# Kernel optimization log

Measured on AMD Instinct MI355X. Metric: run time of the kernel, lower is better.

The kernel has to match this reference:

```python
import jax, jax.numpy as jnp
import numpy as np
import math

N, E = 50000, 800000
N_BASIS, N_ATOM, L = 32, 128, 2
START, STOP = 0.0, 10.0

_idx = [(i, j, L - i - j) for i in range(L + 1) for j in range(L + 1 - i)]
IP = np.array([t[0] for t in _idx], np.float32)
JP = np.array([t[1] for t in _idx], np.float32)
KP = np.array([t[2] for t in _idx], np.float32)
_d = np.array([math.factorial(a) * math.factorial(b) * math.factorial(c) for a, b, c in _idx], np.float32)
PREF2 = np.sqrt(math.factorial(L) / _d).astype(np.float32)  # [T], T = (L+1)(L+2)/2 = 6
OFFSETS = np.linspace(START, STOP, N_BASIS, dtype=np.float32)
WIDTH = np.float32(OFFSETS[1] - OFFSETS[0])


def _signed_pow(x, p):
    # matches torch.pow for negative base with integer-valued float exponent
    p = np.asarray(p)
    odd = (p.astype(np.int64) % 2 == 1)
    r = jnp.abs(x)[:, None] ** jnp.asarray(p)[None, :]
    return jnp.where((x < 0.0)[:, None] & jnp.asarray(odd)[None, :], -r, r)


def setup_inputs() -> dict:
    key = jax.random.key(0)
    ks = jax.random.split(key, 12)
    s = 0.05
    return {
        "feat": jax.random.normal(ks[0], (N, N_ATOM), jnp.float32),
        "dis_vec": jax.random.normal(ks[1], (E, 3), jnp.float32),
        "cj_w1": jax.random.normal(ks[2], (N_ATOM, N_ATOM), jnp.float32) * s,
        "cj_b1": jnp.zeros((N_ATOM,), jnp.float32),
        "cj_w2": jax.random.normal(ks[3], (N_ATOM, 1), jnp.float32) * s,
        "cj_b2": jnp.zeros((1,), jnp.float32),
        "msg_w1": jax.random.normal(ks[4], (N_BASIS, N_ATOM), jnp.float32) * s,
        "msg_b1": jnp.zeros((N_ATOM,), jnp.float32),
        "msg_w2": jax.random.normal(ks[5], (N_ATOM, N_ATOM), jnp.float32) * s,
        "msg_b2": jnp.zeros((N_ATOM,), jnp.float32),
        "filt_w1": jax.random.normal(ks[6], (IP.shape[0], IP.shape[0]), jnp.float32) * s,
        "filt_w2": jax.random.normal(ks[7], (IP.shape[0], 1), jnp.float32) * s,
        "filt_b2": jnp.zeros((1,), jnp.float32),
        "src": jax.random.randint(ks[8], (E,), 0, N, jnp.int32),
        "dst": jax.random.randint(ks[9], (E,), 0, N, jnp.int32),
    }


def reference(feat, dis_vec, cj_w1, cj_b1, cj_w2, cj_b2, msg_w1, msg_b1, msg_w2, msg_b2, filt_w1, filt_w2, filt_b2, src, dst):
    silu = jax.nn.silu  # swish
    # polynomial prefactor: [E, T]
    phix = _signed_pow(dis_vec[:, 0] + 1e-8, IP)
    phiy = _signed_pow(dis_vec[:, 1] + 1e-8, JP)
    phiz = _signed_pow(dis_vec[:, 2] + 1e-8, KP)
    prefactor = phix * phiy * phiz
    # gaussian basis: [E, n_basis] (cutoff_network is None -> C = 1)
    dis = jnp.linalg.norm(dis_vec + 1e-9, axis=-1)
    coeff = -0.5 / (WIDTH ** 2)
    g0 = jnp.exp(coeff * (dis[:, None] - jnp.asarray(OFFSETS)[None, :]) ** 2)
    # gauss: [E, n_basis, T]
    gauss = prefactor[:, None, :] * g0[:, :, None] * jnp.asarray(PREF2)[None, None, :]
    # cj = cj_mlp(feat): [N, 1]
    cj = silu(feat @ cj_w1 + cj_b1) @ cj_w2 + cj_b2
    # e_mul_v: gather dst-node scalar onto edges; copy_e_sum(g.reverse()): scatter-sum to src nodes
    fij = gauss * cj[dst][:, :, None]  # [E, n_basis, T]
    agg = jax.ops.segment_sum(fij, src, num_segments=N)  # [N, n_basis, T]
    f2 = jnp.sum(agg ** 2, axis=-1)  # [N, n_basis]
    msg_in = f2 / (jnp.linalg.norm(f2 + 1e-9, axis=-1, keepdims=True) + 1.0)
    msg_out = silu(msg_in @ msg_w1 + msg_b1) @ msg_w2 + msg_b2  # [N, n_atom_basis]
    gn = gauss / (jnp.linalg.norm(gauss + 1e-8, axis=-1) + 1.0)[..., None]
    filt = (silu(gn @ filt_w1) @ filt_w2 + filt_b2)[..., 0]  # [E, n_basis]
    return msg_out, filt
```

## Files before the change

kernel.cpp:

```cpp
#include <hip/hip_runtime.h>
#include <math.h>

#define N_NODES 50000
#define N_EDGES 800000
#define NB 32
#define NA 128
#define CJ_BLOCKS 782
#define CNT_BLOCKS 3125
#define EDGE_BLOCKS 3125
#define SCAN_BLOCKS 49

constexpr double STEP_D = 10.0 / 31.0;
constexpr float  STEP_F = (float)(10.0 / 31.0);
constexpr float  COEFF  = -0.5f / (STEP_F * STEP_F);
constexpr float  R2     = 1.41421356237309515f;
constexpr float  INV_STEP = 3.1f;
constexpr float  HWIN   = 2.05f;

__device__ __forceinline__ float fast_rcp(float x) {
    return __builtin_amdgcn_rcpf(x);
}

__device__ __forceinline__ float silu_f(float x) {
    return x * fast_rcp(1.0f + __expf(-x));
}

__global__ __launch_bounds__(256) void k_cj_count(const float* __restrict__ feat,
                                                  const float* __restrict__ w1,
                                                  const float* __restrict__ b1,
                                                  const float* __restrict__ w2,
                                                  const float* __restrict__ b2,
                                                  float* __restrict__ cj,
                                                  const int* __restrict__ src,
                                                  int* __restrict__ cnt) {
    __shared__ float fls[64 * 128];
    int tid = threadIdx.x;
    int blk = blockIdx.x;
    if (blk >= CJ_BLOCKS) {
        int e = (blk - CJ_BLOCKS) * 256 + tid;
        if (e < N_EDGES) atomicAdd(&cnt[src[e]], 1);
        return;
    }
    int jq  = tid & 31;
    int ng  = tid >> 5;
    int j0  = jq * 4;
    int n0  = blk * 64;

    {
        const float4* fp = (const float4*)feat;
        int base = n0 * 32;
        int maxi = N_NODES * 32 - 1;
#pragma unroll
        for (int r = 0; r < 8; r++) {
            int idx = base + r * 256 + tid;
            ((float4*)fls)[r * 256 + tid] = fp[min(idx, maxi)];
        }
    }
    __syncthreads();

    float4 bv = *(const float4*)&b1[j0];
    float h[8][4];
#pragma unroll
    for (int i = 0; i < 8; i++) {
        h[i][0] = bv.x; h[i][1] = bv.y; h[i][2] = bv.z; h[i][3] = bv.w;
    }
    for (int kb = 0; kb < 128; kb += 4) {
        float4 wv[4];
#pragma unroll
        for (int u = 0; u < 4; u++) wv[u] = *(const float4*)&w1[(kb + u) * 128 + j0];
#pragma unroll
        for (int i = 0; i < 8; i++) {
            float4 f4 = *(const float4*)&fls[(ng * 8 + i) * 128 + kb];
            h[i][0] = fmaf(f4.x, wv[0].x, h[i][0]);
            h[i][1] = fmaf(f4.x, wv[0].y, h[i][1]);
            h[i][2] = fmaf(f4.x, wv[0].z, h[i][2]);
            h[i][3] = fmaf(f4.x, wv[0].w, h[i][3]);
            h[i][0] = fmaf(f4.y, wv[1].x, h[i][0]);
            h[i][1] = fmaf(f4.y, wv[1].y, h[i][1]);
            h[i][2] = fmaf(f4.y, wv[1].z, h[i][2]);
            h[i][3] = fmaf(f4.y, wv[1].w, h[i][3]);
            h[i][0] = fmaf(f4.z, wv[2].x, h[i][0]);
            h[i][1] = fmaf(f4.z, wv[2].y, h[i][1]);
            h[i][2] = fmaf(f4.z, wv[2].z, h[i][2]);
            h[i][3] = fmaf(f4.z, wv[2].w, h[i][3]);
            h[i][0] = fmaf(f4.w, wv[3].x, h[i][0]);
            h[i][1] = fmaf(f4.w, wv[3].y, h[i][1]);
            h[i][2] = fmaf(f4.w, wv[3].z, h[i][2]);
            h[i][3] = fmaf(f4.w, wv[3].w, h[i][3]);
        }
    }
    float4 w2v = *(const float4*)&w2[j0];
    float keep = 0.f;
#pragma unroll
    for (int i = 0; i < 8; i++) {
        float v = silu_f(h[i][0]) * w2v.x + silu_f(h[i][1]) * w2v.y
                + silu_f(h[i][2]) * w2v.z + silu_f(h[i][3]) * w2v.w;
#pragma unroll
        for (int m = 1; m < 32; m <<= 1) v += __shfl_xor(v, m, 64);
        if (jq == i) keep = v;
    }
    if (jq < 8) {
        int n = n0 + ng * 8 + jq;
        if (n < N_NODES) cj[n] = b2[0] + keep;
    }
}

__global__ __launch_bounds__(1024) void k_scan(const int* __restrict__ cnt,
                                               int* __restrict__ offs,
                                               int* __restrict__ cursor,
                                               int* __restrict__ bsum) {
    __shared__ int s[1024];
    __shared__ int sbase;
    int bid = blockIdx.x;
    int i = bid * 1024 + threadIdx.x;
    int v = (i < N_NODES) ? cnt[i] : 0;
    s[threadIdx.x] = v;
    __syncthreads();
    for (int o = 1; o < 1024; o <<= 1) {
        int t = (threadIdx.x >= (unsigned)o) ? s[threadIdx.x - o] : 0;
        __syncthreads();
        s[threadIdx.x] += t;
        __syncthreads();
    }
    if (threadIdx.x == 1023) atomicExch(&bsum[bid], s[1023] + 1);
    if (threadIdx.x < 64) {
        int lane = threadIdx.x;
        int val = 0;
        if (lane < bid) {
            int t;
            do { t = atomicAdd(&bsum[lane], 0); } while (t == 0);
            val = t - 1;
        }
#pragma unroll
        for (int m = 1; m < 64; m <<= 1) val += __shfl_xor(val, m, 64);
        if (lane == 0) sbase = val;
    }
    __syncthreads();
    if (i < N_NODES) {
        int o2 = s[threadIdx.x] - v + sbase;
        offs[i] = o2;
        cursor[i] = o2;
    }
}

__global__ __launch_bounds__(256) void k_edge(const int* __restrict__ src,
                                              const int* __restrict__ dst,
                                              const float* __restrict__ dis_vec,
                                              const float* __restrict__ cj,
                                              int* __restrict__ cursor,
                                              float* __restrict__ sedge,
                                              const float* __restrict__ fw1,
                                              const float* __restrict__ fw2,
                                              const float* __restrict__ fb2,
                                              float* __restrict__ outf) {
    __shared__ float buf[256 * 36];
    int tid = threadIdx.x;
    int e = blockIdx.x * 256 + tid;
    int se = src[e];
    int de = dst[e];
    float dx = dis_vec[3 * e], dy = dis_vec[3 * e + 1], dz = dis_vec[3 * e + 2];
    float cjd = cj[de];
    int p = atomicAdd(&cursor[se], 1);

    float ax = dx + 1e-9f, ay = dy + 1e-9f, az = dz + 1e-9f;
    float dis = sqrtf(ax * ax + ay * ay + az * az);
    float x = dx + 1e-8f, y = dy + 1e-8f, z = dz + 1e-8f;
    float pre[6];
    pre[0] = z * z;      pre[1] = y * z * R2; pre[2] = y * y;
    pre[3] = x * z * R2; pre[4] = x * y * R2; pre[5] = x * x;

    {
        float4* op = (float4*)(sedge + (size_t)p * 8);
        op[0] = make_float4(dis, pre[0] * cjd, pre[1] * cjd, pre[2] * cjd);
        op[1] = make_float4(pre[3] * cjd, pre[4] * cjd, pre[5] * cjd, 0.f);
    }

    float A = 0.f, B = 0.f;
#pragma unroll
    for (int t = 0; t < 6; t++) { A = fmaf(pre[t], pre[t], A); B += pre[t]; }
    float q[6];
#pragma unroll
    for (int tp = 0; tp < 6; tp++) {
        float s = 0.f;
#pragma unroll
        for (int t = 0; t < 6; t++) s = fmaf(pre[t], fw1[t * 6 + tp], s);
        q[tp] = s;
    }
    float bias = fb2[0];
    float w2r[6];
#pragma unroll
    for (int t = 0; t < 6; t++) w2r[t] = fw2[t];

    float* row = &buf[tid * 36];
    float4 b4v = make_float4(bias, bias, bias, bias);
#pragma unroll
    for (int r = 0; r < 8; r++) ((float4*)row)[r] = b4v;

    int b_lo = (int)ceilf((dis - HWIN) * INV_STEP);
#pragma unroll
    for (int k = 0; k < 14; k++) {
        int b = b_lo + k;
        float offb = (float)((double)b * STEP_D);
        float dd = dis - offb;
        float g = __expf(COEFF * dd * dd);
        float ns = fmaf(g * g, A, fmaf(2e-8f * g, B, 6e-16f));
        float rn = fast_rcp(sqrtf(ns) + 1.0f);
        float s = g * rn;
        float o = bias;
#pragma unroll
        for (int tp = 0; tp < 6; tp++) o = fmaf(silu_f(s * q[tp]), w2r[tp], o);
        if ((unsigned)b < 32u) row[b] = o;
    }
    __syncthreads();

    float4* ob = (float4*)(outf + (size_t)blockIdx.x * (256 * 32));
#pragma unroll
    for (int r = 0; r < 8; r++) {
        int g = r * 256 + tid;
        int eloc = g >> 3, j = g & 7;
        ob[g] = *(const float4*)&buf[eloc * 36 + j * 4];
    }
}

__global__ __launch_bounds__(256) void k_agg(const float* __restrict__ sedge,
                                             const int* __restrict__ offs,
                                             const int* __restrict__ cnt,
                                             float* __restrict__ msg_in) {
    int lane = threadIdx.x & 63;
    int n = blockIdx.x * 4 + (threadIdx.x >> 6);
    if (n >= N_NODES) return;
    int b = lane >> 1, th = lane & 1;
    float offb = (float)((double)b * STEP_D);
    int beg = offs[n];
    int deg = cnt[n];
    const float4* sp = (const float4*)sedge + (size_t)beg * 2;
    float a0 = 0.f, a1 = 0.f, a2 = 0.f;
    int i = 0;
    for (; i + 8 <= deg; i += 8) {
        float4 r[16];
#pragma unroll
        for (int u = 0; u < 16; u++) r[u] = sp[u];
        sp += 16;
#pragma unroll
        for (int u = 0; u < 8; u++) {
            float4 r0 = r[2 * u], r1 = r[2 * u + 1];
            float dd = r0.x - offb;
            float g = __expf(COEFF * dd * dd);
            float w0 = th ? r1.x : r0.y;
            float w1 = th ? r1.y : r0.z;
            float w2 = th ? r1.z : r0.w;
            a0 = fmaf(g, w0, a0);
            a1 = fmaf(g, w1, a1);
            a2 = fmaf(g, w2, a2);
        }
    }
    for (; i < deg; i++) {
        float4 r0 = sp[0], r1 = sp[1];
        sp += 2;
        float dd = r0.x - offb;
        float g = __expf(COEFF * dd * dd);
        float w0 = th ? r1.x : r0.y;
        float w1 = th ? r1.y : r0.z;
        float w2 = th ? r1.z : r0.w;
        a0 = fmaf(g, w0, a0);
        a1 = fmaf(g, w1, a1);
        a2 = fmaf(g, w2, a2);
    }
    float s = a0 * a0 + a1 * a1 + a2 * a2;
    float f2 = s + __shfl_xor(s, 1, 64);
    float p = f2 + 1e-9f;
    p = p * p;
    float tot = p;
#pragma unroll
    for (int m = 1; m < 64; m <<= 1) tot += __shfl_xor(tot, m, 64);
    float nrm = sqrtf(0.5f * tot);
    float val = f2 * fast_rcp(nrm + 1.0f);
    if (th == 0) msg_in[(size_t)n * NB + b] = val;
}

__global__ __launch_bounds__(256) void k_msg(const float* __restrict__ msg_in,
                                             const float* __restrict__ w1,
                                             const float* __restrict__ b1,
                                             const float* __restrict__ w2,
                                             const float* __restrict__ b2,
                                             float* __restrict__ out) {
    __shared__ float mi[64 * 32];
    __shared__ float sh[64 * 128];
    int tid = threadIdx.x;
    int jq  = tid & 31;
    int ng  = tid >> 5;
    int j0  = jq * 4;
    int n0  = blockIdx.x * 64;

    {
        const float4* srcp = (const float4*)msg_in;
        int base = n0 * 8;
        int maxi = N_NODES * 8 - 1;
#pragma unroll
        for (int r = 0; r < 2; r++) {
            int idx = base + r * 256 + tid;
            ((float4*)mi)[r * 256 + tid] = srcp[min(idx, maxi)];
        }
    }
    __syncthreads();

    float4 b1v = *(const float4*)&b1[j0];
    float h[8][4];
#pragma unroll
    for (int i = 0; i < 8; i++) {
        h[i][0] = b1v.x; h[i][1] = b1v.y; h[i][2] = b1v.z; h[i][3] = b1v.w;
    }
#pragma unroll
    for (int bb = 0; bb < 32; bb += 4) {
        float4 wv[4];
#pragma unroll
        for (int u = 0; u < 4; u++) wv[u] = *(const float4*)&w1[(bb + u) * 128 + j0];
#pragma unroll
        for (int i = 0; i < 8; i++) {
            float4 m4 = *(const float4*)&mi[(ng * 8 + i) * 32 + bb];
            h[i][0] = fmaf(m4.x, wv[0].x, h[i][0]);
            h[i][1] = fmaf(m4.x, wv[0].y, h[i][1]);
            h[i][2] = fmaf(m4.x, wv[0].z, h[i][2]);
            h[i][3] = fmaf(m4.x, wv[0].w, h[i][3]);
            h[i][0] = fmaf(m4.y, wv[1].x, h[i][0]);
            h[i][1] = fmaf(m4.y, wv[1].y, h[i][1]);
            h[i][2] = fmaf(m4.y, wv[1].z, h[i][2]);
            h[i][3] = fmaf(m4.y, wv[1].w, h[i][3]);
            h[i][0] = fmaf(m4.z, wv[2].x, h[i][0]);
            h[i][1] = fmaf(m4.z, wv[2].y, h[i][1]);
            h[i][2] = fmaf(m4.z, wv[2].z, h[i][2]);
            h[i][3] = fmaf(m4.z, wv[2].w, h[i][3]);
            h[i][0] = fmaf(m4.w, wv[3].x, h[i][0]);
            h[i][1] = fmaf(m4.w, wv[3].y, h[i][1]);
            h[i][2] = fmaf(m4.w, wv[3].z, h[i][2]);
            h[i][3] = fmaf(m4.w, wv[3].w, h[i][3]);
        }
    }
#pragma unroll
    for (int i = 0; i < 8; i++) {
        float4 sv = make_float4(silu_f(h[i][0]), silu_f(h[i][1]),
                                silu_f(h[i][2]), silu_f(h[i][3]));
        *(float4*)&sh[(ng * 8 + i) * 128 + j0] = sv;
    }
    __syncthreads();

    float4 b2v = *(const float4*)&b2[j0];
    float acc[8][4];
#pragma unroll
    for (int i = 0; i < 8; i++) {
        acc[i][0] = b2v.x; acc[i][1] = b2v.y; acc[i][2] = b2v.z; acc[i][3] = b2v.w;
    }
    for (int hb = 0; hb < 128; hb += 4) {
        float4 wv[4];
#pragma unroll
        for (int u = 0; u < 4; u++) wv[u] = *(const float4*)&w2[(hb + u) * 128 + j0];
#pragma unroll
        for (int i = 0; i < 8; i++) {
            float4 s4 = *(const float4*)&sh[(ng * 8 + i) * 128 + hb];
            acc[i][0] = fmaf(s4.x, wv[0].x, acc[i][0]);
            acc[i][1] = fmaf(s4.x, wv[0].y, acc[i][1]);
            acc[i][2] = fmaf(s4.x, wv[0].z, acc[i][2]);
            acc[i][3] = fmaf(s4.x, wv[0].w, acc[i][3]);
            acc[i][0] = fmaf(s4.y, wv[1].x, acc[i][0]);
            acc[i][1] = fmaf(s4.y, wv[1].y, acc[i][1]);
            acc[i][2] = fmaf(s4.y, wv[1].z, acc[i][2]);
            acc[i][3] = fmaf(s4.y, wv[1].w, acc[i][3]);
            acc[i][0] = fmaf(s4.z, wv[2].x, acc[i][0]);
            acc[i][1] = fmaf(s4.z, wv[2].y, acc[i][1]);
            acc[i][2] = fmaf(s4.z, wv[2].z, acc[i][2]);
            acc[i][3] = fmaf(s4.z, wv[2].w, acc[i][3]);
            acc[i][0] = fmaf(s4.w, wv[3].x, acc[i][0]);
            acc[i][1] = fmaf(s4.w, wv[3].y, acc[i][1]);
            acc[i][2] = fmaf(s4.w, wv[3].z, acc[i][2]);
            acc[i][3] = fmaf(s4.w, wv[3].w, acc[i][3]);
        }
    }
#pragma unroll
    for (int i = 0; i < 8; i++) {
        int n = n0 + ng * 8 + i;
        if (n < N_NODES) {
            *(float4*)&out[(size_t)n * 128 + j0] =
                make_float4(acc[i][0], acc[i][1], acc[i][2], acc[i][3]);
        }
    }
}

extern "C" void kernel_launch(void* const* d_in, const int* in_sizes, int n_in,
                              void* d_out, int out_size, void* d_ws, size_t ws_size,
                              hipStream_t stream) {
    (void)in_sizes; (void)n_in; (void)out_size; (void)ws_size;
    const float* feat    = (const float*)d_in[0];
    const float* dis_vec = (const float*)d_in[1];
    const float* cj_w1   = (const float*)d_in[2];
    const float* cj_b1   = (const float*)d_in[3];
    const float* cj_w2   = (const float*)d_in[4];
    const float* cj_b2   = (const float*)d_in[5];
    const float* msg_w1  = (const float*)d_in[6];
    const float* msg_b1  = (const float*)d_in[7];
    const float* msg_w2  = (const float*)d_in[8];
    const float* msg_b2  = (const float*)d_in[9];
    const float* filt_w1 = (const float*)d_in[10];
    const float* filt_w2 = (const float*)d_in[11];
    const float* filt_b2 = (const float*)d_in[12];
    const int*   src     = (const int*)d_in[13];
    const int*   dst     = (const int*)d_in[14];
    float* out = (float*)d_out;

    float* ws     = (float*)d_ws;
    float* cj     = ws;
    int*   cnt    = (int*)(cj + 50048);
    int*   bsum   = cnt + 50048;
    int*   offs   = bsum + 64;
    int*   cursor = offs + 50048;
    float* msg_in = (float*)(cursor + 50048);
    float* sedge  = msg_in + 1600256;

    hipMemsetAsync(cnt, 0, (50048 + 64) * sizeof(int), stream);

    k_cj_count<<<CJ_BLOCKS + CNT_BLOCKS, 256, 0, stream>>>(feat, cj_w1, cj_b1, cj_w2,
                                                           cj_b2, cj, src, cnt);
    k_scan<<<SCAN_BLOCKS, 1024, 0, stream>>>(cnt, offs, cursor, bsum);
    k_edge<<<EDGE_BLOCKS, 256, 0, stream>>>(src, dst, dis_vec, cj, cursor, sedge,
                                            filt_w1, filt_w2, filt_b2,
                                            out + (size_t)N_NODES * NA);
    k_agg<<<(N_NODES + 3) / 4, 256, 0, stream>>>(sedge, offs, cnt, msg_in);
    k_msg<<<(N_NODES + 63) / 64, 256, 0, stream>>>(msg_in, msg_w1, msg_b1, msg_w2, msg_b2, out);
}
```

Before: 350.6 us.

## Split edge filter work across 8 lanes per edge with shuffle output

The edge kernel now assigns 8 threads to each edge instead of one. Each lane computes 2 of the 14 Gaussian window bins, and the results are redistributed with wavefront shuffles so every lane writes one float4 of the 32-wide output row. This drops the LDS staging buffer and the block barrier, and raises parallelism to 25000 blocks. In exchange, the per-edge setup work (norm, prefactors, the 6x6 matvec) is done redundantly by all 8 lanes, and only lane 0 does the atomic cursor update and the sedge write.

```diff
diff --git a/kernel.cpp b/kernel.cpp
--- a/kernel.cpp
+++ b/kernel.cpp
@@ -7,7 +7,7 @@
 #define NA 128
 #define CJ_BLOCKS 782
 #define CNT_BLOCKS 3125
-#define EDGE_BLOCKS 3125
+#define EDGE_BLOCKS 25000
 #define SCAN_BLOCKS 49
 
 constexpr double STEP_D = 10.0 / 31.0;
@@ -153,15 +153,13 @@
                                               const float* __restrict__ fw2,
                                               const float* __restrict__ fb2,
                                               float* __restrict__ outf) {
-    __shared__ float buf[256 * 36];
     int tid = threadIdx.x;
-    int e = blockIdx.x * 256 + tid;
-    int se = src[e];
-    int de = dst[e];
+    int lane = tid & 63;
+    int j = lane & 7;
+    int g0 = lane & 56;
+    int e = blockIdx.x * 32 + (tid >> 3);
+
     float dx = dis_vec[3 * e], dy = dis_vec[3 * e + 1], dz = dis_vec[3 * e + 2];
-    float cjd = cj[de];
-    int p = atomicAdd(&cursor[se], 1);
-
     float ax = dx + 1e-9f, ay = dy + 1e-9f, az = dz + 1e-9f;
     float dis = sqrtf(ax * ax + ay * ay + az * az);
     float x = dx + 1e-8f, y = dy + 1e-8f, z = dz + 1e-8f;
@@ -169,7 +167,11 @@
     pre[0] = z * z;      pre[1] = y * z * R2; pre[2] = y * y;
     pre[3] = x * z * R2; pre[4] = x * y * R2; pre[5] = x * x;
 
-    {
+    if (j == 0) {
+        int se = src[e];
+        int de = dst[e];
+        float cjd = cj[de];
+        int p = atomicAdd(&cursor[se], 1);
         float4* op = (float4*)(sedge + (size_t)p * 8);
         op[0] = make_float4(dis, pre[0] * cjd, pre[1] * cjd, pre[2] * cjd);
         op[1] = make_float4(pre[3] * cjd, pre[4] * cjd, pre[5] * cjd, 0.f);
@@ -191,35 +193,38 @@
 #pragma unroll
     for (int t = 0; t < 6; t++) w2r[t] = fw2[t];
 
-    float* row = &buf[tid * 36];
-    float4 b4v = make_float4(bias, bias, bias, bias);
-#pragma unroll
-    for (int r = 0; r < 8; r++) ((float4*)row)[r] = b4v;
-
     int b_lo = (int)ceilf((dis - HWIN) * INV_STEP);
-#pragma unroll
-    for (int k = 0; k < 14; k++) {
-        int b = b_lo + k;
-        float offb = (float)((double)b * STEP_D);
+
+    float os[2];
+#pragma unroll
+    for (int u = 0; u < 2; u++) {
+        int s = 2 * j + u;
+        float offb = (float)((double)(b_lo + s) * STEP_D);
         float dd = dis - offb;
         float g = __expf(COEFF * dd * dd);
         float ns = fmaf(g * g, A, fmaf(2e-8f * g, B, 6e-16f));
         float rn = fast_rcp(sqrtf(ns) + 1.0f);
-        float s = g * rn;
+        float sg = g * rn;
         float o = bias;
 #pragma unroll
-        for (int tp = 0; tp < 6; tp++) o = fmaf(silu_f(s * q[tp]), w2r[tp], o);
-        if ((unsigned)b < 32u) row[b] = o;
-    }
-    __syncthreads();
-
-    float4* ob = (float4*)(outf + (size_t)blockIdx.x * (256 * 32));
-#pragma unroll
-    for (int r = 0; r < 8; r++) {
-        int g = r * 256 + tid;
-        int eloc = g >> 3, j = g & 7;
-        ob[g] = *(const float4*)&buf[eloc * 36 + j * 4];
-    }
+        for (int tp = 0; tp < 6; tp++) o = fmaf(silu_f(sg * q[tp]), w2r[tp], o);
+        os[u] = o;
+    }
+
+    float res[4];
+#pragma unroll
+    for (int t = 0; t < 4; t++) {
+        int b = 4 * j + t;
+        int st = b - b_lo;
+        int stc = min(max(st, 0), 13);
+        int sl = g0 + (stc >> 1);
+        float v0 = __shfl(os[0], sl, 64);
+        float v1 = __shfl(os[1], sl, 64);
+        float v = (stc & 1) ? v1 : v0;
+        res[t] = ((unsigned)st < 14u) ? v : bias;
+    }
+    *(float4*)&outf[(size_t)e * 32 + 4 * j] =
+        make_float4(res[0], res[1], res[2], res[3]);
 }
 
 __global__ __launch_bounds__(256) void k_agg(const float* __restrict__ sedge,
```

After: 375.4 us. +7.1%, slower.
